# Optimization experiments

Measured on AMD Instinct MI355X. Metric: run time of the kernel, lower is better.

The kernel has to match this reference:

```python
import jax, jax.numpy as jnp
import numpy as np

VOCAB, EMB, HID, TEMP = 10000, 256, 512, 0.5
EPS = 1e-20


def _lstm(x_seq, h0, c0, Wih, Whh, b):
    # x_seq: [T, B, E]; PyTorch gate order i, f, g, o
    def step(carry, x):
        h, c = carry
        gates = x @ Wih + h @ Whh + b
        i, f, g, o = jnp.split(gates, 4, axis=-1)
        c = jax.nn.sigmoid(f) * c + jax.nn.sigmoid(i) * jnp.tanh(g)
        h = jax.nn.sigmoid(o) * jnp.tanh(c)
        return (h, c), h
    (hT, cT), hs = jax.lax.scan(step, (h0, c0), x_seq)
    return hs, hT, cT


def setup_inputs() -> dict:
    key = jax.random.key(0)
    ks = jax.random.split(key, 16)
    B, T = 32, 128
    s = 0.02
    input_ids = jax.random.randint(ks[0], (B, T), 0, VOCAB, dtype=jnp.int32)
    mask = jax.random.randint(ks[1], (B, T), 0, 2, dtype=jnp.int32)
    U = jax.random.uniform(ks[2], (T, B, VOCAB), dtype=jnp.float32)
    gumbel_noise = -jnp.log(-jnp.log(U + EPS) + EPS)
    return {
        'input_ids': input_ids,
        'my_attention_mask': mask,
        'enc_embed': s * jax.random.normal(ks[3], (VOCAB, EMB), jnp.float32),
        'enc_Wih': s * jax.random.normal(ks[4], (EMB, 4 * HID), jnp.float32),
        'enc_Whh': s * jax.random.normal(ks[5], (HID, 4 * HID), jnp.float32),
        'enc_b': jnp.zeros((4 * HID,), jnp.float32),
        'dec_embed': s * jax.random.normal(ks[6], (VOCAB, EMB), jnp.float32),
        'dec_Wih': s * jax.random.normal(ks[7], (EMB, 4 * HID), jnp.float32),
        'dec_Whh': s * jax.random.normal(ks[8], (HID, 4 * HID), jnp.float32),
        'dec_b': jnp.zeros((4 * HID,), jnp.float32),
        'fc_W': s * jax.random.normal(ks[9], (HID, VOCAB), jnp.float32),
        'fc_b': jnp.zeros((VOCAB,), jnp.float32),
        'rand_init': jax.random.uniform(ks[10], (T, B, VOCAB), dtype=jnp.float32),
        'gumbel_noise': gumbel_noise,
    }


def reference(input_ids, my_attention_mask, enc_embed, enc_Wih, enc_Whh, enc_b,
              dec_embed, dec_Wih, dec_Whh, dec_b, fc_W, fc_b,
              rand_init, gumbel_noise):
    B, T = input_ids.shape
    mask = my_attention_mask                      # [B, T]
    tokens = input_ids.T                          # [T, B] (torch.t of view)

    h0 = jnp.zeros((B, HID), jnp.float32)
    # Encoder over full sequence
    _, hT, cT = _lstm(enc_embed[tokens], h0, h0, enc_Wih, enc_Whh, enc_b)
    # Decoder: teacher-forced on tokens[0:T-1] -> outputs for steps t=1..T-1
    hs, _, _ = _lstm(dec_embed[tokens[:-1]], hT, cT, dec_Wih, dec_Whh, dec_b)
    logits = hs @ fc_W + fc_b                     # [T-1, B, V]

    # Mask-driven compaction: outputs[sum(mask[j,:t]), j] = logits[t-1, j] where mask[j,t]==1
    excl = jnp.cumsum(mask, axis=1) - mask        # exclusive prefix sum [B, T]
    pos = excl[:, 1:]                             # [B, T-1]
    valid = mask[:, 1:] > 0
    pos_use = jnp.where(valid, pos, T)            # out-of-range -> dropped
    jj = jnp.broadcast_to(jnp.arange(B)[:, None], pos_use.shape)
    outputs = rand_init.at[pos_use, jj].set(jnp.swapaxes(logits, 0, 1), mode='drop')  # [T, B, V]

    # Hard gumbel-softmax with straight-through
    y = jax.nn.softmax((outputs + gumbel_noise) / TEMP, axis=-1)
    y_hard = jax.nn.one_hot(jnp.argmax(y, axis=-1), VOCAB, dtype=y.dtype)
    gs = jax.lax.stop_gradient(y_hard - y) + y    # [T, B, V]

    # Re-expand: masked positions take compacted gumbel rows, unmasked take token one-hots
    gathered = gs[excl, jnp.arange(B)[:, None]]   # [B, T, V]
    tok_oh = jax.nn.one_hot(input_ids, VOCAB, dtype=jnp.float32)
    onehots = jnp.where((mask > 0)[..., None], gathered, tok_oh)  # [B, T, V]
    return onehots.reshape(-1, VOCAB)             # dense form of the sparse inputs_embeds
```

## Files before the change

### kernel.cpp

```cpp
#include <hip/hip_runtime.h>
#include <hip/hip_bf16.h>
#include <math.h>

#define BB 32
#define TT 128
#define TD 127
#define EMB 256
#define HID 512
#define G4 2048
#define NV 10000
#define NB 64
#define NWK 192
#define GRID_UBER (NB + NWK)
#define UPB 8
#define NT_STEPS (TT + TD)
#define CAND_CAP 16
#define CAND_DELTA 1.0f

#define NJOB_DEC 512
#define NJOB_TR  313
#define NJOB_WN  20
#define NJOB_RM  4096
#define NJOBS (NJOB_DEC + NJOB_TR + NJOB_WN + NJOB_RM)

typedef __attribute__((ext_vector_type(8))) short short8v;
typedef __attribute__((ext_vector_type(4))) float f32x4;

__device__ __forceinline__ unsigned short bf16_rne(float x){
    unsigned int u = __float_as_uint(x);
    u += 0x7fffu + ((u >> 16) & 1u);
    return (unsigned short)(u >> 16);
}
__device__ __forceinline__ float bf16f(unsigned short h){
    return __uint_as_float(((unsigned int)h) << 16);
}

__global__ __launch_bounds__(256) void gemm_x(const int* __restrict__ ids,
        const float* __restrict__ embed, const float* __restrict__ W,
        const float* __restrict__ bias, float* __restrict__ X, int M)
{
    __shared__ float As[16][128];
    __shared__ float Bs[16][128];
    __shared__ int toks[128];
    const int tid = threadIdx.x;
    const int m0 = blockIdx.y * 128, n0 = blockIdx.x * 128;
    if (tid < 128) {
        int mr = m0 + tid, tk = 0;
        if (mr < M) { int t = mr >> 5, b = mr & 31; tk = ids[b*TT + t]; }
        toks[tid] = tk;
    }
    __syncthreads();
    float acc[8][8] = {};
    const int ty = tid >> 4, tx = tid & 15;
    for (int kt = 0; kt < EMB; kt += 16) {
        #pragma unroll
        for (int i = 0; i < 2; i++) {
            int idx = tid*2 + i;
            int row = idx >> 2, k4 = (idx & 3)*4;
            float4 a = *(const float4*)&embed[(size_t)toks[row]*EMB + kt + k4];
            As[k4+0][row] = a.x; As[k4+1][row] = a.y; As[k4+2][row] = a.z; As[k4+3][row] = a.w;
        }
        #pragma unroll
        for (int i = 0; i < 2; i++) {
            int idx = tid*2 + i;
            int kr = idx >> 5, c4 = (idx & 31)*4;
            *(float4*)&Bs[kr][c4] = *(const float4*)&W[(size_t)(kt+kr)*G4 + n0 + c4];
        }
        __syncthreads();
        #pragma unroll
        for (int k = 0; k < 16; k++) {
            float a8[8], b8[8];
            #pragma unroll
            for (int i = 0; i < 8; i++) a8[i] = As[k][ty*8+i];
            #pragma unroll
            for (int j = 0; j < 8; j++) b8[j] = Bs[k][tx*8+j];
            #pragma unroll
            for (int i = 0; i < 8; i++) {
                #pragma unroll
                for (int j = 0; j < 8; j++)
                    acc[i][j] = fmaf(a8[i], b8[j], acc[i][j]);
            }
        }
        __syncthreads();
    }
    #pragma unroll
    for (int i = 0; i < 8; i++) {
        int mr = m0 + ty*8 + i;
        if (mr < M) {
            int tt = mr >> 5, bb2 = mr & 31;
            #pragma unroll
            for (int j = 0; j < 8; j++) {
                int nc = n0 + tx*8 + j;
                X[((size_t)tt*G4 + nc)*BB + bb2] = acc[i][j] + bias[nc];
            }
        }
    }
}

__global__ __launch_bounds__(512) void lstm_persist(
        const float* __restrict__ Xenc, float* __restrict__ Xdec,
        const float* __restrict__ Whh_e, const float* __restrict__ Whh_d,
        unsigned int* __restrict__ h_pk,
        float* __restrict__ hs,
        int* __restrict__ flags,
        int* __restrict__ decdone,
        const int* __restrict__ ids, const float* __restrict__ dEmb,
        const float* __restrict__ dWih, const float* __restrict__ dB,
        const float* __restrict__ fcW, float* __restrict__ fcWt,
        const float* __restrict__ fcb, const int* __restrict__ mask,
        const float* __restrict__ gum, const float* __restrict__ rinit,
        float* __restrict__ Mr, unsigned int* __restrict__ scal,
        int* __restrict__ candCnt, int* __restrict__ candList,
        float* __restrict__ outp)
{
    __shared__ float smem[11392];
    const int tid = threadIdx.x;
    const int bid = blockIdx.x;

    if (bid >= NB) {
        const int wid = bid - NB;
        for (int job = wid; job < NJOBS; job += NWK) {
            if (job < NJOB_DEC) {
                const int my = job >> 4, nx = job & 15;
                const int m0 = my*128, n0 = nx*128;
                const int M = TD*BB;
                float* As = smem;
                float* Bs = smem + 2048;
                int* toks = (int*)(smem + 4096);
                if (tid < 128) {
                    int mr = m0 + tid, tk = 0;
                    if (mr < M) { int t = mr >> 5, b2 = mr & 31; tk = ids[b2*TT + t]; }
                    toks[tid] = tk;
                }
                __syncthreads();
                float acc[4][8] = {};
                const int ty = tid >> 4, tx = tid & 15;
                for (int kt = 0; kt < EMB; kt += 16) {
                    {
                        int row = tid >> 2, k4 = (tid & 3)*4;
                        float4 a = *(const float4*)&dEmb[(size_t)toks[row]*EMB + kt + k4];
                        As[(k4+0)*128+row] = a.x; As[(k4+1)*128+row] = a.y;
                        As[(k4+2)*128+row] = a.z; As[(k4+3)*128+row] = a.w;
                    }
                    {
                        int kr = tid >> 5, c4 = (tid & 31)*4;
                        *(float4*)&Bs[kr*128 + c4] =
                            *(const float4*)&dWih[(size_t)(kt+kr)*G4 + n0 + c4];
                    }
                    __syncthreads();
                    #pragma unroll
                    for (int k = 0; k < 16; k++) {
                        float a4[4], b8[8];
                        #pragma unroll
                        for (int i = 0; i < 4; i++) a4[i] = As[k*128 + ty*4+i];
                        #pragma unroll
                        for (int j = 0; j < 8; j++) b8[j] = Bs[k*128 + tx*8+j];
                        #pragma unroll
                        for (int i = 0; i < 4; i++) {
                            #pragma unroll
                            for (int j = 0; j < 8; j++)
                                acc[i][j] = fmaf(a4[i], b8[j], acc[i][j]);
                        }
                    }
                    __syncthreads();
                }
                #pragma unroll
                for (int i = 0; i < 4; i++) {
                    int mr = m0 + ty*4 + i;
                    if (mr < M) {
                        int t = mr >> 5, b2 = mr & 31;
                        #pragma unroll
                        for (int j = 0; j < 8; j++) {
                            int nc = n0 + tx*8 + j;
                            Xdec[((size_t)t*G4 + nc)*BB + b2] = acc[i][j] + dB[nc];
                        }
                    }
                }
                __syncthreads();
                if (tid == 0)
                    __hip_atomic_fetch_add(decdone, 1,
                        __ATOMIC_RELEASE, __HIP_MEMORY_SCOPE_AGENT);
            } else if (job < NJOB_DEC + NJOB_TR) {
                const int v0 = (job - NJOB_DEC)*32;
                float* tile = smem;
                for (int k0 = 0; k0 < HID; k0 += 16) {
                    {
                        int kk = tid >> 5, vv = tid & 31;
                        int v = v0 + vv;
                        tile[kk*33 + vv] = (v < NV) ? fcW[(size_t)(k0+kk)*NV + v] : 0.f;
                    }
                    __syncthreads();
                    {
                        int vy = tid >> 4, kx = tid & 15;
                        int v = v0 + vy;
                        if (v < NV) fcWt[(size_t)v*HID + k0 + kx] = tile[kx*33 + vy];
                    }
                    __syncthreads();
                }
            } else if (job < NJOB_DEC + NJOB_TR + NJOB_WN) {
                int v = (job - NJOB_DEC - NJOB_TR)*512 + tid;
                if (v < NV) {
                    float s = 0.f;
                    for (int k = 0; k < HID; k++) {
                        float x = fcW[(size_t)k*NV + v]; s = fmaf(x, x, s);
                    }
                    atomicMax(&scal[0], __float_as_uint(s));
                    atomicMax(&scal[1], __float_as_uint(fabsf(fcb[v])));
                }
            } else {
                const int row = job - NJOB_DEC - NJOB_TR - NJOB_WN;
                const int b = row >> 7, t = row & 127;
                const int mrow = mask[row];
                float4* o = (float4*)(outp + (size_t)row*NV);
                if (mrow == 0) {
                    int win = ids[b*TT + t];
                    for (int idx = tid; idx < 2500; idx += 512) {
                        int vb = idx*4;
                        float4 val = {0.f,0.f,0.f,0.f};
                        if (win >= vb && win < vb+4) ((float*)&val)[win-vb] = 1.0f;
                        o[idx] = val;
                    }
                } else if (t == 0) {
                    const float* g  = gum   + (size_t)b*NV;
                    const float* r0 = rinit + (size_t)b*NV;
                    float bs = -1e30f; int bv = 0x7fffffff;
                    for (int v = tid; v < NV; v += 512) {
                        float sc = r0[v] + g[v];
                        if (sc > bs || (sc == bs && v < bv)) { bs = sc; bv = v; }
                    }
                    float* red = smem;
                    int* idxr = (int*)(smem + 512);
                    red[tid] = bs; idxr[tid] = bv; __syncthreads();
                    for (int s = 256; s; s >>= 1) {
                        if (tid < s) {
                            if (red[tid+s] > red[tid] ||
                                (red[tid+s] == red[tid] && idxr[tid+s] < idxr[tid])) {
                                red[tid] = red[tid+s]; idxr[tid] = idxr[tid+s];
                            }
                        }
                        __syncthreads();
                    }
                    int win = idxr[0];
                    __syncthreads();
                    for (int idx = tid; idx < 2500; idx += 512) {
                        int vb = idx*4;
                        float4 val = {0.f,0.f,0.f,0.f};
                        if (win >= vb && win < vb+4) ((float*)&val)[win-vb] = 1.0f;
                        o[idx] = val;
                    }
                } else {
                    int* wk   = (int*)&smem[1024];
                    int* ccnt = (int*)&smem[1040];
                    int mi = (tid < TT) ? mask[b*TT + tid] : 0;
                    unsigned long long bal = __ballot(tid < t && mi != 0);
                    if ((tid & 63) == 0) wk[tid >> 6] = __popcll(bal);
                    if (tid == 0) *ccnt = 0;
                    __syncthreads();
                    const int k = wk[0] + wk[1];
                    const float* g = gum + ((size_t)k*BB + b)*NV;
                    float m = -1e30f;
                    for (int v = tid; v < NV; v += 512) m = fmaxf(m, g[v]);
                    float* red = smem;
                    red[tid] = m; __syncthreads();
                    for (int s = 256; s; s >>= 1) {
                        if (tid < s) red[tid] = fmaxf(red[tid], red[tid+s]);
                        __syncthreads();
                    }
                    const float Mv = red[0];
                    const float thr0 = Mv - CAND_DELTA;
                    for (int v = tid; v < NV; v += 512) {
                        if (g[v] >= thr0) {
                            int pos = atomicAdd(ccnt, 1);
                            if (pos < CAND_CAP) candList[row*CAND_CAP + pos] = v;
                        }
                    }
                    float4 z = {0.f,0.f,0.f,0.f};
                    for (int idx = tid; idx < 2500; idx += 512) o[idx] = z;
                    __syncthreads();
                    if (tid == 0) { candCnt[row] = *ccnt; Mr[row] = Mv; }
                    __syncthreads();
                }
            }
        }
        return;
    }

    float* partials = smem;
    float* xbuf     = smem + 9216;

    const int u0  = bid*UPB;
    const int w   = tid >> 6;
    const int l   = tid & 63;
    const int rl  = l & 15;
    const int kg  = (l >> 4) * 8;
    const int r4  = (l >> 4) * 4;
    const int gb  = tid >> 3, gul = tid & 7;

    short8v wH_n0k0, wH_n0k1, wH_n1k0, wH_n1k1;
    short8v wL_n0k0, wL_n0k1, wL_n1k0, wL_n1k1;

    #define BW(WH, WL, KB, CO) do { _Pragma("unroll") \
        for (int j = 0; j < 8; ++j) { \
            float wv2 = partials[((KB)+j)*32 + (CO) + rl]; \
            unsigned short htop = bf16_rne(wv2); \
            WH[j] = (short)htop; \
            WL[j] = (short)bf16_rne(wv2 - bf16f(htop)); \
        } } while(0)

    #define STAGE_BUILD(SRC) do { \
        for (int c = 0; c < 4; ++c) { \
            int k0 = c*128; \
            __syncthreads(); \
            for (int i = tid; i < 4096; i += 512) { \
                int kl = i >> 5, n = i & 31; \
                partials[kl*32 + n] = SRC[(size_t)(k0+kl)*G4 + (size_t)((n>>3)*512 + u0 + (n&7))]; \
            } \
            __syncthreads(); \
            if ((w >> 1) == c) { \
                int kb0 = w*64 - k0 + kg; \
                BW(wH_n0k0, wL_n0k0, kb0,      0); \
                BW(wH_n0k1, wL_n0k1, kb0 + 32, 0); \
                BW(wH_n1k0, wL_n1k0, kb0,     16); \
                BW(wH_n1k1, wL_n1k1, kb0 + 32,16); \
            } \
        } \
        __syncthreads(); } while(0)

    STAGE_BUILD(Whh_e);

    {
        for (int i = tid; i < 1024; i += 512) {
            int row2 = i & 31, n = i >> 5;
            xbuf[row2*33 + n] = Xenc[(size_t)((n>>3)*512 + u0 + (n&7))*32 + row2];
        }
        __syncthreads();
    }

    float c_reg = 0.f;

    #define MM6(ACC, AH0, AH1, AL0, AL1, WH0, WH1, WL0, WL1) do { \
        ACC = __builtin_amdgcn_mfma_f32_16x16x32_bf16(AH0, WH0, ACC, 0,0,0); \
        ACC = __builtin_amdgcn_mfma_f32_16x16x32_bf16(AH1, WH1, ACC, 0,0,0); \
        ACC = __builtin_amdgcn_mfma_f32_16x16x32_bf16(AL0, WH0, ACC, 0,0,0); \
        ACC = __builtin_amdgcn_mfma_f32_16x16x32_bf16(AL1, WH1, ACC, 0,0,0); \
        ACC = __builtin_amdgcn_mfma_f32_16x16x32_bf16(AH0, WL0, ACC, 0,0,0); \
        ACC = __builtin_amdgcn_mfma_f32_16x16x32_bf16(AH1, WL1, ACC, 0,0,0); \
    } while(0)

    for (int gstep = 0; gstep < NT_STEPS; ++gstep) {
        const bool enc = gstep < TT;
        const int t = enc ? gstep : gstep - TT;

        f32x4 acc00 = {0,0,0,0}, acc01 = {0,0,0,0}, acc10 = {0,0,0,0}, acc11 = {0,0,0,0};
        if (gstep > 0) {
            const unsigned int* hp = h_pk + (size_t)(gstep & 1)*16384;
            short8v aH_m0k0, aH_m0k1, aH_m1k0, aH_m1k1;
            short8v aL_m0k0, aL_m0k1, aL_m1k0, aL_m1k1;
            #define LOAD_A(AH, AL, MT, KS) do { \
                unsigned int pv[8]; \
                int kbase = w*64 + (KS)*32 + kg; \
                int brow = (MT)*16 + rl; \
                _Pragma("unroll") \
                for (int j = 0; j < 8; ++j) \
                    pv[j] = __hip_atomic_load(&hp[(kbase+j)*32 + brow], \
                                __ATOMIC_RELAXED, __HIP_MEMORY_SCOPE_AGENT); \
                _Pragma("unroll") \
                for (int j = 0; j < 8; ++j) { \
                    AH[j] = (short)(pv[j] & 0xffffu); \
                    AL[j] = (short)(pv[j] >> 16); \
                } } while(0)
            LOAD_A(aH_m0k0, aL_m0k0, 0, 0); LOAD_A(aH_m0k1, aL_m0k1, 0, 1);
            LOAD_A(aH_m1k0, aL_m1k0, 1, 0); LOAD_A(aH_m1k1, aL_m1k1, 1, 1);
            MM6(acc00, aH_m0k0, aH_m0k1, aL_m0k0, aL_m0k1, wH_n0k0, wH_n0k1, wL_n0k0, wL_n0k1);
            MM6(acc01, aH_m0k0, aH_m0k1, aL_m0k0, aL_m0k1, wH_n1k0, wH_n1k1, wL_n1k0, wL_n1k1);
            MM6(acc10, aH_m1k0, aH_m1k1, aL_m1k0, aL_m1k1, wH_n0k0, wH_n0k1, wL_n0k0, wL_n0k1);
            MM6(acc11, aH_m1k0, aH_m1k1, aL_m1k0, aL_m1k1, wH_n1k0, wH_n1k1, wL_n1k0, wL_n1k1);
        }
        #pragma unroll
        for (int j = 0; j < 4; ++j) {
            partials[(w*32 +      r4 + j)*36 +      rl] = acc00[j];
            partials[(w*32 +      r4 + j)*36 + 16 + rl] = acc01[j];
            partials[(w*32 + 16 + r4 + j)*36 +      rl] = acc10[j];
            partials[(w*32 + 16 + r4 + j)*36 + 16 + rl] = acc11[j];
        }
        __syncthreads();

        float hv = 0.f;
        if (tid < 256) {
            float pre[4];
            #pragma unroll
            for (int gg = 0; gg < 4; ++gg) {
                float s = xbuf[(gstep & 1)*1056 + gb*33 + gg*8 + gul];
                #pragma unroll
                for (int ww = 0; ww < 8; ++ww)
                    s += partials[(ww*32 + gb)*36 + gg*8 + gul];
                pre[gg] = s;
            }
            float iv = 1.f/(1.f + expf(-pre[0]));
            float fv = 1.f/(1.f + expf(-pre[1]));
            float gv = tanhf(pre[2]);
            float ov = 1.f/(1.f + expf(-pre[3]));
            c_reg = fmaf(fv, c_reg, iv*gv);
            hv = ov * tanhf(c_reg);
            unsigned short hh = bf16_rne(hv);
            unsigned short hl = bf16_rne(hv - bf16f(hh));
            unsigned int pk = (unsigned int)hh | ((unsigned int)hl << 16);
            __hip_atomic_store(&h_pk[(size_t)((gstep+1) & 1)*16384 + (u0+gul)*32 + gb],
                               pk, __ATOMIC_RELAXED, __HIP_MEMORY_SCOPE_AGENT);
        }
        __syncthreads();
        if (gstep < NT_STEPS - 1 && tid == 0)
            __hip_atomic_store(&flags[bid], gstep + 1,
                               __ATOMIC_RELAXED, __HIP_MEMORY_SCOPE_AGENT);
        if (!enc && tid < 256)
            hs[((size_t)t*BB + gb)*HID + u0 + gul] = hv;
        if (gstep == NT_STEPS - 1) break;

        if (gstep == TT - 1) STAGE_BUILD(Whh_d);

        {
            if (gstep + 1 == TT) {
                if (tid == 0) {
                    while (__hip_atomic_load(decdone, __ATOMIC_RELAXED,
                                             __HIP_MEMORY_SCOPE_AGENT) < NJOB_DEC)
                        __builtin_amdgcn_s_sleep(8);
                }
                __syncthreads();
                __builtin_amdgcn_fence(__ATOMIC_ACQUIRE, "agent");
            }
            int tn = gstep + 1 < TT ? gstep + 1 : gstep + 1 - TT;
            const float* Xt = (gstep + 1 < TT ? Xenc : (const float*)Xdec) + (size_t)tn*G4*BB;
            for (int i = tid; i < 1024; i += 512) {
                int row2 = i & 31, n = i >> 5;
                xbuf[((gstep+1) & 1)*1056 + row2*33 + n] =
                    Xt[(size_t)((n>>3)*512 + u0 + (n&7))*32 + row2];
            }
        }
        if (tid < NB) {
            while (__hip_atomic_load(&flags[tid], __ATOMIC_RELAXED,
                                     __HIP_MEMORY_SCOPE_AGENT) <= gstep) {}
        }
        __syncthreads();
        asm volatile("" ::: "memory");
    }
}

__global__ __launch_bounds__(256) void cand_write(
        const int* __restrict__ mask, const float* __restrict__ gum,
        const float* __restrict__ hs, const float* __restrict__ Wt,
        const float* __restrict__ fcb, const float* __restrict__ Mr,
        const unsigned int* __restrict__ scal,
        const int* __restrict__ candCnt, const int* __restrict__ candList,
        float* __restrict__ out)
{
    const int row = blockIdx.x, b = row >> 7, t = row & 127;
    if (t == 0 || mask[row] == 0) return;
    const int tid = threadIdx.x;
    __shared__ float red[256];
    __shared__ int list[256];
    __shared__ int wcnt[4];

    int mi = (tid < TT) ? mask[b*TT + tid] : 0;
    unsigned long long bal = __ballot(tid < t && mi != 0);
    if ((tid & 63) == 0) wcnt[tid >> 6] = __popcll(bal);
    __syncthreads();
    const int k = wcnt[0] + wcnt[1];
    __syncthreads();

    const float* g    = gum + ((size_t)k*BB + b)*NV;
    const float* hrow = hs + ((size_t)(t-1)*BB + b)*HID;
    float hn = 0.f;
    for (int k2 = tid; k2 < HID; k2 += 256) { float x = hrow[k2]; hn = fmaf(x, x, hn); }
    red[tid] = hn; __syncthreads();
    for (int s = 128; s; s >>= 1) {
        if (tid < s) red[tid] += red[tid+s];
        __syncthreads();
    }
    const float Mv = Mr[row];
    float bound = sqrtf(__uint_as_float(scal[0])) * sqrtf(red[0])
                + __uint_as_float(scal[1]);
    float thr = Mv - 2.0f*bound*1.05f - 1e-6f;
    __syncthreads();

    float curS = -1e30f; int curV = 0x7fffffff;
    const int cnt = candCnt[row];

    if (cnt <= CAND_CAP && thr >= Mv - CAND_DELTA) {
        for (int ci = 0; ci < cnt; ci++) {
            int vc = candList[row*CAND_CAP + ci];
            float p = 0.f;
            for (int k2 = tid; k2 < HID; k2 += 256)
                p = fmaf(hrow[k2], Wt[(size_t)vc*HID + k2], p);
            red[tid] = p; __syncthreads();
            for (int s = 128; s; s >>= 1) {
                if (tid < s) red[tid] += red[tid+s];
                __syncthreads();
            }
            if (tid == 0) {
                float sc = (red[0] + fcb[vc]) + g[vc];
                if (sc > curS || (sc == curS && vc < curV)) { curS = sc; curV = vc; }
            }
            __syncthreads();
        }
    } else {
        int wv = tid >> 6, lane = tid & 63;
        for (int v0 = 0; v0 < NV; v0 += 256) {
            int v = v0 + tid;
            bool ok = (v < NV) && (g[v] >= thr);
            unsigned long long mb = __ballot(ok);
            if (lane == 0) wcnt[wv] = __popcll(mb);
            __syncthreads();
            int off = 0;
            #pragma unroll
            for (int w = 0; w < 4; w++) if (w < wv) off += wcnt[w];
            int tot = wcnt[0] + wcnt[1] + wcnt[2] + wcnt[3];
            if (ok) {
                int pos = off + __popcll(mb & ((1ull << lane) - 1ull));
                list[pos] = v;
            }
            __syncthreads();
            for (int ci = 0; ci < tot; ci++) {
                int vc = list[ci];
                float p = 0.f;
                for (int k2 = tid; k2 < HID; k2 += 256)
                    p = fmaf(hrow[k2], Wt[(size_t)vc*HID + k2], p);
                red[tid] = p; __syncthreads();
                for (int s = 128; s; s >>= 1) {
                    if (tid < s) red[tid] += red[tid+s];
                    __syncthreads();
                }
                if (tid == 0) {
                    float sc = (red[0] + fcb[vc]) + g[vc];
                    if (sc > curS || (sc == curS && vc < curV)) { curS = sc; curV = vc; }
                }
                __syncthreads();
            }
        }
    }
    if (tid == 0) out[(size_t)row*NV + curV] = 1.0f;
}

extern "C" void kernel_launch(void* const* d_in, const int* in_sizes, int n_in,
                              void* d_out, int out_size, void* d_ws, size_t ws_size,
                              hipStream_t stream)
{
    const int*   ids   = (const int*)d_in[0];
    const int*   mask  = (const int*)d_in[1];
    const float* eEmb  = (const float*)d_in[2];
    const float* eWih  = (const float*)d_in[3];
    const float* eWhh  = (const float*)d_in[4];
    const float* eB    = (const float*)d_in[5];
    const float* dEmb  = (const float*)d_in[6];
    const float* dWih  = (const float*)d_in[7];
    const float* dWhh  = (const float*)d_in[8];
    const float* dB    = (const float*)d_in[9];
    const float* fcW   = (const float*)d_in[10];
    const float* fcb   = (const float*)d_in[11];
    const float* rinit = (const float*)d_in[12];
    const float* gum   = (const float*)d_in[13];
    float* out = (float*)d_out;

    float* wsf = (float*)d_ws;
    size_t off = 0;
    float* Xenc = wsf + off; off += (size_t)TT*BB*G4;
    float* Xdec = wsf + off; off += (size_t)TD*BB*G4;
    unsigned int* h_pk = (unsigned int*)(wsf + off); off += 2*(size_t)BB*HID;
    float* hs   = wsf + off; off += (size_t)TD*BB*HID;
    float* fcWt = wsf + off; off += (size_t)NV*HID;
    float* Mr   = wsf + off; off += 4096;
    int* candCnt  = (int*)(wsf + off); off += 4096;
    int* candList = (int*)(wsf + off); off += 4096*CAND_CAP;
    unsigned int* ctl = (unsigned int*)(wsf + off); off += 128;
    unsigned int* scal = ctl;
    int* flags   = (int*)(ctl + 8);
    int* decdone = (int*)(ctl + 72);

    hipMemsetAsync(ctl, 0, 128*sizeof(int), stream);

    dim3 gblk(16, 32);
    gemm_x<<<gblk, 256, 0, stream>>>(ids, eEmb, eWih, eB, Xenc, TT*BB);

    lstm_persist<<<GRID_UBER, 512, 0, stream>>>(Xenc, Xdec, eWhh, dWhh,
        h_pk, hs, flags, decdone,
        ids, dEmb, dWih, dB, fcW, fcWt, fcb, mask, gum, rinit,
        Mr, scal, candCnt, candList, out);

    cand_write<<<4096, 256, 0, stream>>>(mask, gum, hs, fcWt, fcb,
                                         Mr, scal, candCnt, candList, out);
}
```

Measured before the change: 967.9 us.

## Specialize warps in LSTM step loop to cut barriers and overlap flag polling

Splits the persistent LSTM block's per-step work across wavefronts. Waves 1-4 compute gates and publish h, and wave 1 raises the block flag once an LDS counter shows all four gate waves have finished their stores. Wave 0 polls the other blocks' flags with a ballot, and waves 5-7 prefetch the next step's input projection. This replaces three __syncthreads per step with one raw s_barrier plus explicit waitcnts, and moves the decoder weight restage to the start of the step. The intent is to shorten the serial per-timestep critical path, at the cost of relying on relaxed atomics and s_waitcnt ordering rather than full fences between the h stores and the flag store.

Result: slower. 1.556 ms (+60.7%).

```diff
diff --git a/kernel.cpp b/kernel.cpp
--- a/kernel.cpp
+++ b/kernel.cpp
@@ -114,6 +114,7 @@
         float* __restrict__ outp)
 {
     __shared__ float smem[11392];
+    __shared__ int gdone;
     const int tid = threadIdx.x;
     const int bid = blockIdx.x;
 
@@ -294,7 +295,8 @@
     const int rl  = l & 15;
     const int kg  = (l >> 4) * 8;
     const int r4  = (l >> 4) * 4;
-    const int gb  = tid >> 3, gul = tid & 7;
+    const int gtid = tid - 64;
+    const int gb  = gtid >> 3, gul = gtid & 7;
 
     short8v wH_n0k0, wH_n0k1, wH_n1k0, wH_n1k1;
     short8v wL_n0k0, wL_n0k1, wL_n1k0, wL_n1k1;
@@ -329,6 +331,7 @@
     STAGE_BUILD(Whh_e);
 
     {
+        if (tid == 0) gdone = 0;
         for (int i = tid; i < 1024; i += 512) {
             int row2 = i & 31, n = i >> 5;
             xbuf[row2*33 + n] = Xenc[(size_t)((n>>3)*512 + u0 + (n&7))*32 + row2];
@@ -349,7 +352,8 @@
 
     for (int gstep = 0; gstep < NT_STEPS; ++gstep) {
         const bool enc = gstep < TT;
-        const int t = enc ? gstep : gstep - TT;
+        const bool last = (gstep == NT_STEPS - 1);
+        if (gstep == TT) STAGE_BUILD(Whh_d);
 
         f32x4 acc00 = {0,0,0,0}, acc01 = {0,0,0,0}, acc10 = {0,0,0,0}, acc11 = {0,0,0,0};
         if (gstep > 0) {
@@ -383,10 +387,10 @@
             partials[(w*32 + 16 + r4 + j)*36 +      rl] = acc10[j];
             partials[(w*32 + 16 + r4 + j)*36 + 16 + rl] = acc11[j];
         }
-        __syncthreads();
-
-        float hv = 0.f;
-        if (tid < 256) {
+        asm volatile("s_waitcnt lgkmcnt(0)" ::: "memory");
+        __builtin_amdgcn_s_barrier();
+
+        if (w >= 1 && w <= 4) {
             float pre[4];
             #pragma unroll
             for (int gg = 0; gg < 4; ++gg) {
@@ -401,46 +405,52 @@
             float gv = tanhf(pre[2]);
             float ov = 1.f/(1.f + expf(-pre[3]));
             c_reg = fmaf(fv, c_reg, iv*gv);
-            hv = ov * tanhf(c_reg);
+            float hv = ov * tanhf(c_reg);
             unsigned short hh = bf16_rne(hv);
             unsigned short hl = bf16_rne(hv - bf16f(hh));
             unsigned int pk = (unsigned int)hh | ((unsigned int)hl << 16);
+            if (!enc) hs[((size_t)(gstep-TT)*BB + gb)*HID + u0 + gul] = hv;
             __hip_atomic_store(&h_pk[(size_t)((gstep+1) & 1)*16384 + (u0+gul)*32 + gb],
                                pk, __ATOMIC_RELAXED, __HIP_MEMORY_SCOPE_AGENT);
-        }
-        __syncthreads();
-        if (gstep < NT_STEPS - 1 && tid == 0)
-            __hip_atomic_store(&flags[bid], gstep + 1,
-                               __ATOMIC_RELAXED, __HIP_MEMORY_SCOPE_AGENT);
-        if (!enc && tid < 256)
-            hs[((size_t)t*BB + gb)*HID + u0 + gul] = hv;
-        if (gstep == NT_STEPS - 1) break;
-
-        if (gstep == TT - 1) STAGE_BUILD(Whh_d);
-
-        {
-            if (gstep + 1 == TT) {
-                if (tid == 0) {
+            asm volatile("s_waitcnt vmcnt(0)" ::: "memory");
+            if (!last) {
+                if (l == 0) atomicAdd(&gdone, 1);
+                if (w == 1) {
+                    int tgt = 4*(gstep + 1);
+                    while (*(volatile int*)&gdone < tgt) {}
+                    if (l == 0)
+                        __hip_atomic_store(&flags[bid], gstep + 1,
+                                           __ATOMIC_RELAXED, __HIP_MEMORY_SCOPE_AGENT);
+                }
+            }
+        } else if (w == 0) {
+            if (!last) {
+                while (true) {
+                    int f = __hip_atomic_load(&flags[l], __ATOMIC_RELAXED,
+                                              __HIP_MEMORY_SCOPE_AGENT);
+                    if (__ballot(f <= gstep) == 0ull) break;
+                }
+            }
+        } else {
+            if (!last) {
+                if (gstep + 1 == TT) {
                     while (__hip_atomic_load(decdone, __ATOMIC_RELAXED,
                                              __HIP_MEMORY_SCOPE_AGENT) < NJOB_DEC)
                         __builtin_amdgcn_s_sleep(8);
-                }
-                __syncthreads();
-                __builtin_amdgcn_fence(__ATOMIC_ACQUIRE, "agent");
-            }
-            int tn = gstep + 1 < TT ? gstep + 1 : gstep + 1 - TT;
-            const float* Xt = (gstep + 1 < TT ? Xenc : (const float*)Xdec) + (size_t)tn*G4*BB;
-            for (int i = tid; i < 1024; i += 512) {
-                int row2 = i & 31, n = i >> 5;
-                xbuf[((gstep+1) & 1)*1056 + row2*33 + n] =
-                    Xt[(size_t)((n>>3)*512 + u0 + (n&7))*32 + row2];
-            }
-        }
-        if (tid < NB) {
-            while (__hip_atomic_load(&flags[tid], __ATOMIC_RELAXED,
-                                     __HIP_MEMORY_SCOPE_AGENT) <= gstep) {}
-        }
-        __syncthreads();
+                    __builtin_amdgcn_fence(__ATOMIC_ACQUIRE, "agent");
+                }
+                int tn = gstep + 1 < TT ? gstep + 1 : gstep + 1 - TT;
+                const float* Xt = (gstep + 1 < TT ? Xenc : (const float*)Xdec)
+                                  + (size_t)tn*G4*BB;
+                for (int i = tid - 320; i < 1024; i += 192) {
+                    int row2 = i & 31, n = i >> 5;
+                    xbuf[((gstep+1) & 1)*1056 + row2*33 + n] =
+                        Xt[(size_t)((n>>3)*512 + u0 + (n&7))*32 + row2];
+                }
+            }
+        }
+        asm volatile("s_waitcnt lgkmcnt(0)" ::: "memory");
+        __builtin_amdgcn_s_barrier();
         asm volatile("" ::: "memory");
     }
 }
```

## Fold encoder input GEMM into persistent kernel with per-row-block readiness flags

Applied to the files above, without the earlier changes.

Removes the separate gemm_x launch and computes the encoder input projection as worker jobs inside the persistent LSTM kernel. Each 128-row block (four timesteps) signals completion through its own encdone counter, and the recurrent blocks wait only on the counter for the timestep they need next. The encoder recurrence can therefore start as soon as the first row block is ready instead of waiting for the whole GEMM. The cost is extra spin-waits in the recurrent loop, and throughput now depends on worker blocks producing encoder rows ahead of the recurrence.

New measurement: 1.023 ms. 1.06x slower.

```diff
diff --git a/kernel.cpp b/kernel.cpp
--- a/kernel.cpp
+++ b/kernel.cpp
@@ -17,11 +17,12 @@
 #define CAND_CAP 16
 #define CAND_DELTA 1.0f
 
+#define NJOB_ENC 512
 #define NJOB_DEC 512
 #define NJOB_TR  313
 #define NJOB_WN  20
 #define NJOB_RM  4096
-#define NJOBS (NJOB_DEC + NJOB_TR + NJOB_WN + NJOB_RM)
+#define NJOBS (NJOB_ENC + NJOB_DEC + NJOB_TR + NJOB_WN + NJOB_RM)
 
 typedef __attribute__((ext_vector_type(8))) short short8v;
 typedef __attribute__((ext_vector_type(4))) float f32x4;
@@ -35,77 +36,19 @@
     return __uint_as_float(((unsigned int)h) << 16);
 }
 
-__global__ __launch_bounds__(256) void gemm_x(const int* __restrict__ ids,
-        const float* __restrict__ embed, const float* __restrict__ W,
-        const float* __restrict__ bias, float* __restrict__ X, int M)
-{
-    __shared__ float As[16][128];
-    __shared__ float Bs[16][128];
-    __shared__ int toks[128];
-    const int tid = threadIdx.x;
-    const int m0 = blockIdx.y * 128, n0 = blockIdx.x * 128;
-    if (tid < 128) {
-        int mr = m0 + tid, tk = 0;
-        if (mr < M) { int t = mr >> 5, b = mr & 31; tk = ids[b*TT + t]; }
-        toks[tid] = tk;
-    }
-    __syncthreads();
-    float acc[8][8] = {};
-    const int ty = tid >> 4, tx = tid & 15;
-    for (int kt = 0; kt < EMB; kt += 16) {
-        #pragma unroll
-        for (int i = 0; i < 2; i++) {
-            int idx = tid*2 + i;
-            int row = idx >> 2, k4 = (idx & 3)*4;
-            float4 a = *(const float4*)&embed[(size_t)toks[row]*EMB + kt + k4];
-            As[k4+0][row] = a.x; As[k4+1][row] = a.y; As[k4+2][row] = a.z; As[k4+3][row] = a.w;
-        }
-        #pragma unroll
-        for (int i = 0; i < 2; i++) {
-            int idx = tid*2 + i;
-            int kr = idx >> 5, c4 = (idx & 31)*4;
-            *(float4*)&Bs[kr][c4] = *(const float4*)&W[(size_t)(kt+kr)*G4 + n0 + c4];
-        }
-        __syncthreads();
-        #pragma unroll
-        for (int k = 0; k < 16; k++) {
-            float a8[8], b8[8];
-            #pragma unroll
-            for (int i = 0; i < 8; i++) a8[i] = As[k][ty*8+i];
-            #pragma unroll
-            for (int j = 0; j < 8; j++) b8[j] = Bs[k][tx*8+j];
-            #pragma unroll
-            for (int i = 0; i < 8; i++) {
-                #pragma unroll
-                for (int j = 0; j < 8; j++)
-                    acc[i][j] = fmaf(a8[i], b8[j], acc[i][j]);
-            }
-        }
-        __syncthreads();
-    }
-    #pragma unroll
-    for (int i = 0; i < 8; i++) {
-        int mr = m0 + ty*8 + i;
-        if (mr < M) {
-            int tt = mr >> 5, bb2 = mr & 31;
-            #pragma unroll
-            for (int j = 0; j < 8; j++) {
-                int nc = n0 + tx*8 + j;
-                X[((size_t)tt*G4 + nc)*BB + bb2] = acc[i][j] + bias[nc];
-            }
-        }
-    }
-}
-
 __global__ __launch_bounds__(512) void lstm_persist(
-        const float* __restrict__ Xenc, float* __restrict__ Xdec,
+        float* __restrict__ Xenc, float* __restrict__ Xdec,
         const float* __restrict__ Whh_e, const float* __restrict__ Whh_d,
         unsigned int* __restrict__ h_pk,
         float* __restrict__ hs,
         int* __restrict__ flags,
         int* __restrict__ decdone,
-        const int* __restrict__ ids, const float* __restrict__ dEmb,
-        const float* __restrict__ dWih, const float* __restrict__ dB,
+        int* __restrict__ encdone,
+        const int* __restrict__ ids,
+        const float* __restrict__ eEmb, const float* __restrict__ eWih,
+        const float* __restrict__ eB,
+        const float* __restrict__ dEmb, const float* __restrict__ dWih,
+        const float* __restrict__ dB,
         const float* __restrict__ fcW, float* __restrict__ fcWt,
         const float* __restrict__ fcb, const int* __restrict__ mask,
         const float* __restrict__ gum, const float* __restrict__ rinit,
@@ -120,10 +63,16 @@
     if (bid >= NB) {
         const int wid = bid - NB;
         for (int job = wid; job < NJOBS; job += NWK) {
-            if (job < NJOB_DEC) {
-                const int my = job >> 4, nx = job & 15;
+            if (job < NJOB_ENC + NJOB_DEC) {
+                const bool isenc = job < NJOB_ENC;
+                const int jj = isenc ? job : job - NJOB_ENC;
+                const int my = jj >> 4, nx = jj & 15;
                 const int m0 = my*128, n0 = nx*128;
-                const int M = TD*BB;
+                const int M = isenc ? TT*BB : TD*BB;
+                const float* emb = isenc ? eEmb : dEmb;
+                const float* Wih = isenc ? eWih : dWih;
+                const float* bv  = isenc ? eB   : dB;
+                float* Xo        = isenc ? Xenc : Xdec;
                 float* As = smem;
                 float* Bs = smem + 2048;
                 int* toks = (int*)(smem + 4096);
@@ -138,14 +87,14 @@
                 for (int kt = 0; kt < EMB; kt += 16) {
                     {
                         int row = tid >> 2, k4 = (tid & 3)*4;
-                        float4 a = *(const float4*)&dEmb[(size_t)toks[row]*EMB + kt + k4];
+                        float4 a = *(const float4*)&emb[(size_t)toks[row]*EMB + kt + k4];
                         As[(k4+0)*128+row] = a.x; As[(k4+1)*128+row] = a.y;
                         As[(k4+2)*128+row] = a.z; As[(k4+3)*128+row] = a.w;
                     }
                     {
                         int kr = tid >> 5, c4 = (tid & 31)*4;
                         *(float4*)&Bs[kr*128 + c4] =
-                            *(const float4*)&dWih[(size_t)(kt+kr)*G4 + n0 + c4];
+                            *(const float4*)&Wih[(size_t)(kt+kr)*G4 + n0 + c4];
                     }
                     __syncthreads();
                     #pragma unroll
@@ -172,16 +121,21 @@
                         #pragma unroll
                         for (int j = 0; j < 8; j++) {
                             int nc = n0 + tx*8 + j;
-                            Xdec[((size_t)t*G4 + nc)*BB + b2] = acc[i][j] + dB[nc];
+                            Xo[((size_t)t*G4 + nc)*BB + b2] = acc[i][j] + bv[nc];
                         }
                     }
                 }
                 __syncthreads();
-                if (tid == 0)
-                    __hip_atomic_fetch_add(decdone, 1,
-                        __ATOMIC_RELEASE, __HIP_MEMORY_SCOPE_AGENT);
-            } else if (job < NJOB_DEC + NJOB_TR) {
-                const int v0 = (job - NJOB_DEC)*32;
+                if (tid == 0) {
+                    if (isenc)
+                        __hip_atomic_fetch_add(&encdone[my], 1,
+                            __ATOMIC_RELEASE, __HIP_MEMORY_SCOPE_AGENT);
+                    else
+                        __hip_atomic_fetch_add(decdone, 1,
+                            __ATOMIC_RELEASE, __HIP_MEMORY_SCOPE_AGENT);
+                }
+            } else if (job < NJOB_ENC + NJOB_DEC + NJOB_TR) {
+                const int v0 = (job - NJOB_ENC - NJOB_DEC)*32;
                 float* tile = smem;
                 for (int k0 = 0; k0 < HID; k0 += 16) {
                     {
@@ -197,8 +151,8 @@
                     }
                     __syncthreads();
                 }
-            } else if (job < NJOB_DEC + NJOB_TR + NJOB_WN) {
-                int v = (job - NJOB_DEC - NJOB_TR)*512 + tid;
+            } else if (job < NJOB_ENC + NJOB_DEC + NJOB_TR + NJOB_WN) {
+                int v = (job - NJOB_ENC - NJOB_DEC - NJOB_TR)*512 + tid;
                 if (v < NV) {
                     float s = 0.f;
                     for (int k = 0; k < HID; k++) {
@@ -208,7 +162,7 @@
                     atomicMax(&scal[1], __float_as_uint(fabsf(fcb[v])));
                 }
             } else {
-                const int row = job - NJOB_DEC - NJOB_TR - NJOB_WN;
+                const int row = job - NJOB_ENC - NJOB_DEC - NJOB_TR - NJOB_WN;
                 const int b = row >> 7, t = row & 127;
                 const int mrow = mask[row];
                 float4* o = (float4*)(outp + (size_t)row*NV);
@@ -223,14 +177,14 @@
                 } else if (t == 0) {
                     const float* g  = gum   + (size_t)b*NV;
                     const float* r0 = rinit + (size_t)b*NV;
-                    float bs = -1e30f; int bv = 0x7fffffff;
+                    float bs = -1e30f; int bv2 = 0x7fffffff;
                     for (int v = tid; v < NV; v += 512) {
                         float sc = r0[v] + g[v];
-                        if (sc > bs || (sc == bs && v < bv)) { bs = sc; bv = v; }
+                        if (sc > bs || (sc == bs && v < bv2)) { bs = sc; bv2 = v; }
                     }
                     float* red = smem;
                     int* idxr = (int*)(smem + 512);
-                    red[tid] = bs; idxr[tid] = bv; __syncthreads();
+                    red[tid] = bs; idxr[tid] = bv2; __syncthreads();
                     for (int s = 256; s; s >>= 1) {
                         if (tid < s) {
                             if (red[tid+s] > red[tid] ||
@@ -329,6 +283,9 @@
     STAGE_BUILD(Whh_e);
 
     {
+        while (__hip_atomic_load(&encdone[0], __ATOMIC_RELAXED,
+                                 __HIP_MEMORY_SCOPE_AGENT) < 16)
+            __builtin_amdgcn_s_sleep(2);
         for (int i = tid; i < 1024; i += 512) {
             int row2 = i & 31, n = i >> 5;
             xbuf[row2*33 + n] = Xenc[(size_t)((n>>3)*512 + u0 + (n&7))*32 + row2];
@@ -429,7 +386,13 @@
                 __builtin_amdgcn_fence(__ATOMIC_ACQUIRE, "agent");
             }
             int tn = gstep + 1 < TT ? gstep + 1 : gstep + 1 - TT;
-            const float* Xt = (gstep + 1 < TT ? Xenc : (const float*)Xdec) + (size_t)tn*G4*BB;
+            if (gstep + 1 < TT) {
+                while (__hip_atomic_load(&encdone[tn >> 2], __ATOMIC_RELAXED,
+                                         __HIP_MEMORY_SCOPE_AGENT) < 16)
+                    __builtin_amdgcn_s_sleep(1);
+            }
+            const float* Xt = (gstep + 1 < TT ? (const float*)Xenc : (const float*)Xdec)
+                              + (size_t)tn*G4*BB;
             for (int i = tid; i < 1024; i += 512) {
                 int row2 = i & 31, n = i >> 5;
                 xbuf[((gstep+1) & 1)*1056 + row2*33 + n] =
@@ -572,17 +535,16 @@
     int* candList = (int*)(wsf + off); off += 4096*CAND_CAP;
     unsigned int* ctl = (unsigned int*)(wsf + off); off += 128;
     unsigned int* scal = ctl;
-    int* flags   = (int*)(ctl + 8);
-    int* decdone = (int*)(ctl + 72);
+    int* flags    = (int*)(ctl + 8);
+    int* decdone  = (int*)(ctl + 72);
+    int* encdone  = (int*)(ctl + 80);
 
     hipMemsetAsync(ctl, 0, 128*sizeof(int), stream);
 
-    dim3 gblk(16, 32);
-    gemm_x<<<gblk, 256, 0, stream>>>(ids, eEmb, eWih, eB, Xenc, TT*BB);
-
     lstm_persist<<<GRID_UBER, 512, 0, stream>>>(Xenc, Xdec, eWhh, dWhh,
-        h_pk, hs, flags, decdone,
-        ids, dEmb, dWih, dB, fcW, fcWt, fcb, mask, gum, rinit,
+        h_pk, hs, flags, decdone, encdone,
+        ids, eEmb, eWih, eB, dEmb, dWih, dB,
+        fcW, fcWt, fcb, mask, gum, rinit,
         Mr, scal, candCnt, candList, out);
 
     cand_write<<<4096, 256, 0, stream>>>(mask, gum, hs, fcWt, fcb,
```
